# Optimization experiments

Hardware: AMD Instinct MI355X
Metric: run time of the kernel (lower is better)

Reference implementation:

```python
import jax, jax.numpy as jnp
import numpy as np
import math

NUM_LAYERS = 2
NUM_HEADS = 8
D_MODEL = 256
D_FF = 4 * D_MODEL
FACTOR = 5
B, L, F_IN = 8, 2048, 32


def layer_norm(x, g, b, eps=1e-5):
    m = x.mean(-1, keepdims=True)
    v = ((x - m) ** 2).mean(-1, keepdims=True)
    return (x - m) * jax.lax.rsqrt(v + eps) * g + b


def prob_attention(q, k, v, idx):
    # q,k,v: [B,H,L,Dh]; idx: [L,S] sampled key indices per query (ProbSparse)
    Bq, H, Lq, Dh = q.shape
    u = min(FACTOR * math.ceil(math.log(Lq)), Lq)  # number of 'active' queries
    k_s = k[:, :, idx, :]                              # [B,H,L,S,Dh] gathered keys
    qk_s = jnp.einsum('bhld,bhlsd->bhls', q, k_s)      # sampled scores
    M = qk_s.max(-1) - qk_s.sum(-1) / Lq               # sparsity measure [B,H,L]
    _, top = jax.lax.top_k(M, u)                       # [B,H,u] active query idx
    q_red = jnp.take_along_axis(q, top[..., None], axis=2)   # [B,H,u,Dh]
    scores = jnp.einsum('bhud,bhld->bhul', q_red, k) * (1.0 / math.sqrt(Dh))
    attn = jax.nn.softmax(scores, axis=-1)             # [B,H,u,L]
    upd = jnp.einsum('bhul,bhld->bhud', attn, v)       # [B,H,u,Dh]
    # initial context = mean of V (mask_flag=False), then scatter active rows
    ctx = jnp.broadcast_to(v.mean(2, keepdims=True), (Bq, H, Lq, Dh))
    bi = jnp.arange(Bq)[:, None, None]
    hi = jnp.arange(H)[None, :, None]
    return ctx.at[bi, hi, top].set(upd)


def setup_inputs() -> dict:
    key = jax.random.key(0)
    ks = jax.random.split(key, 16)
    S = min(FACTOR * math.ceil(math.log(L)), L)  # 40
    std = 0.02

    def w(k, shape):
        return jax.random.normal(k, shape, jnp.float32) * std

    inp = {}
    inp['x'] = jax.random.normal(ks[0], (B, L, F_IN), jnp.float32)
    inp['idx_sample'] = jax.random.randint(ks[1], (NUM_LAYERS, L, S), 0, L)
    inp['w_in'] = w(ks[2], (F_IN, D_MODEL)); inp['b_in'] = jnp.zeros((D_MODEL,), jnp.float32)
    inp['wq'] = w(ks[3], (NUM_LAYERS, D_MODEL, D_MODEL)); inp['bq'] = jnp.zeros((NUM_LAYERS, D_MODEL), jnp.float32)
    inp['wk'] = w(ks[4], (NUM_LAYERS, D_MODEL, D_MODEL)); inp['bk'] = jnp.zeros((NUM_LAYERS, D_MODEL), jnp.float32)
    inp['wv'] = w(ks[5], (NUM_LAYERS, D_MODEL, D_MODEL)); inp['bv'] = jnp.zeros((NUM_LAYERS, D_MODEL), jnp.float32)
    inp['wo'] = w(ks[6], (NUM_LAYERS, D_MODEL, D_MODEL)); inp['bo'] = jnp.zeros((NUM_LAYERS, D_MODEL), jnp.float32)
    inp['w_ff1'] = w(ks[7], (NUM_LAYERS, D_MODEL, D_FF)); inp['b_ff1'] = jnp.zeros((NUM_LAYERS, D_FF), jnp.float32)
    inp['w_ff2'] = w(ks[8], (NUM_LAYERS, D_FF, D_MODEL)); inp['b_ff2'] = jnp.zeros((NUM_LAYERS, D_MODEL), jnp.float32)
    inp['ln1_g'] = jnp.ones((NUM_LAYERS, D_MODEL), jnp.float32); inp['ln1_b'] = jnp.zeros((NUM_LAYERS, D_MODEL), jnp.float32)
    inp['ln2_g'] = jnp.ones((NUM_LAYERS, D_MODEL), jnp.float32); inp['ln2_b'] = jnp.zeros((NUM_LAYERS, D_MODEL), jnp.float32)
    inp['w_fc1'] = w(ks[9], (D_MODEL, 64)); inp['b_fc1'] = jnp.zeros((64,), jnp.float32)
    inp['w_fc2'] = w(ks[10], (64, 1)); inp['b_fc2'] = jnp.zeros((1,), jnp.float32)
    return inp


def reference(x, idx_sample, w_in, b_in, wq, bq, wk, bk, wv, bv, wo, bo,
              w_ff1, b_ff1, w_ff2, b_ff2, ln1_g, ln1_b, ln2_g, ln2_b,
              w_fc1, b_fc1, w_fc2, b_fc2):
    Bx, Lx, _ = x.shape
    h = x @ w_in + b_in  # [B,L,D_MODEL]
    for i in range(NUM_LAYERS):
        q = (h @ wq[i] + bq[i]).reshape(Bx, Lx, NUM_HEADS, -1).transpose(0, 2, 1, 3)
        k = (h @ wk[i] + bk[i]).reshape(Bx, Lx, NUM_HEADS, -1).transpose(0, 2, 1, 3)
        v = (h @ wv[i] + bv[i]).reshape(Bx, Lx, NUM_HEADS, -1).transpose(0, 2, 1, 3)
        ctx = prob_attention(q, k, v, idx_sample[i])            # [B,H,L,Dh]
        ctx = ctx.transpose(0, 2, 1, 3).reshape(Bx, Lx, D_MODEL)
        new_x = ctx @ wo[i] + bo[i]
        h = layer_norm(h + new_x, ln1_g[i], ln1_b[i])
        y = jax.nn.relu(h @ w_ff1[i] + b_ff1[i]) @ w_ff2[i] + b_ff2[i]
        h = layer_norm(h + y, ln2_g[i], ln2_b[i])
    last = h[:, -1, :]                      # take final time step
    out = jax.nn.relu(last @ w_fc1 + b_fc1) @ w_fc2 + b_fc2
    return out[:, None, :]                  # unsqueeze(1) -> [B,1,output_size]
```

## Files before the change

kernel.cpp:

```cpp
#include <hip/hip_runtime.h>
#include <math.h>

#define BB 8
#define LL 2048
#define DM 256
#define NH 8
#define DH 32
#define DFF 1024
#define SS 40
#define UU 40
#define BL (BB*LL)
#define NSL 8

#define SCP 260
#define KP  40
#define VP  34

typedef unsigned short ushort_t;
typedef unsigned char uchar_t;
typedef __attribute__((ext_vector_type(8))) short short8;
typedef __attribute__((ext_vector_type(4))) float f32x4;

__device__ inline ushort_t f2b(float f)
{
    unsigned int u = __float_as_uint(f);
    u += 0x7fff + ((u >> 16) & 1);
    return (ushort_t)(u >> 16);
}

__device__ inline float blo(unsigned int u) { return __uint_as_float(u << 16); }
__device__ inline float bhi(unsigned int u) { return __uint_as_float(u & 0xffff0000u); }

__device__ inline void gload16(const void* g, const void* l)
{
    __builtin_amdgcn_global_load_lds(
        (const __attribute__((address_space(1))) unsigned int*)g,
        (__attribute__((address_space(3))) unsigned int*)l, 16, 0, 0);
}

template<int RELU, int OUT_MODE>
__global__ __launch_bounds__(256)
void gemm_mfma(const ushort_t* __restrict__ A, const ushort_t* __restrict__ Bt,
               const float* __restrict__ bias, void* __restrict__ Cout,
               void* __restrict__ aux, int M, int N, int K)
{
    __shared__ ushort_t Asl[128 * 32];
    __shared__ ushort_t Bsl[128 * 32];

    const int t    = threadIdx.x;
    const int lane = t & 63;
    const int wv   = t >> 6;
    const int row0 = blockIdx.x * 128;
    const int col0 = blockIdx.y * 128;
    const int wr   = (wv >> 1) * 64;
    const int wc   = (wv & 1) * 64;
    const int quad = lane >> 4;
    const int l16  = lane & 15;

    f32x4 acc[4][4];
    #pragma unroll
    for (int i = 0; i < 4; ++i)
        #pragma unroll
        for (int j = 0; j < 4; ++j)
            acc[i][j] = 0.f;

    for (int k0 = 0; k0 < K; k0 += 32) {
        __syncthreads();
        #pragma unroll
        for (int r = 0; r < 2; ++r) {
            int g = r * 256 + t;
            const ushort_t* ga = A  + (size_t)(row0 + (g >> 2)) * K + k0 + (g & 3) * 8;
            const ushort_t* gb = Bt + (size_t)(col0 + (g >> 2)) * K + k0 + (g & 3) * 8;
            int lbase = (r * 256 + wv * 64) * 16;
            gload16(ga, (const char*)Asl + lbase);
            gload16(gb, (const char*)Bsl + lbase);
        }
        __syncthreads();

        short8 af[4], bfr[4];
        #pragma unroll
        for (int mi = 0; mi < 4; ++mi)
            af[mi] = *(const short8*)&Asl[(wr + mi * 16 + l16) * 32 + quad * 8];
        #pragma unroll
        for (int ni = 0; ni < 4; ++ni)
            bfr[ni] = *(const short8*)&Bsl[(wc + ni * 16 + l16) * 32 + quad * 8];
        #pragma unroll
        for (int mi = 0; mi < 4; ++mi)
            #pragma unroll
            for (int ni = 0; ni < 4; ++ni)
                acc[mi][ni] = __builtin_amdgcn_mfma_f32_16x16x32_bf16(
                    af[mi], bfr[ni], acc[mi][ni], 0, 0, 0);
    }

    #pragma unroll
    for (int mi = 0; mi < 4; ++mi) {
        #pragma unroll
        for (int ni = 0; ni < 4; ++ni) {
            int col = col0 + wc + ni * 16 + l16;
            float bb = bias[col];
            #pragma unroll
            for (int r = 0; r < 4; ++r) {
                int row = row0 + wr + mi * 16 + quad * 4 + r;
                float v = acc[mi][ni][r] + bb;
                if (RELU) v = v > 0.f ? v : 0.f;
                if (OUT_MODE == 0) {
                    ((float*)Cout)[(size_t)row * N + col] = v;
                } else if (OUT_MODE == 1) {
                    int tensor = col >> 8;
                    int c2 = col & 255;
                    int b  = row >> 11, l = row & (LL - 1);
                    int hh = c2 >> 5,  dh = c2 & 31;
                    int bh = b * NH + hh;
                    size_t bi = (((size_t)bh * LL + l) << 5) + dh;
                    ushort_t vb16 = f2b(v);
                    ((ushort_t*)Cout)[(size_t)tensor * (BB*NH*LL*DH) + bi] = vb16;
                    if (tensor == 1)
                        ((ushort_t*)aux)[(((size_t)l << 6) + bh) * 32 + dh] = vb16;
                } else if (OUT_MODE == 2) {
                    ((ushort_t*)Cout)[(size_t)row * N + col] = f2b(v);
                } else {
                    ((float*)Cout)[(size_t)row * N + col] = v;
                    ((ushort_t*)aux)[(size_t)row * N + col] = f2b(v);
                }
            }
        }
    }
}

template<int HEAD>
__global__ __launch_bounds__(256)
void gemmln_k(const ushort_t* __restrict__ A, const ushort_t* __restrict__ Bt,
              const float* __restrict__ bias, float* __restrict__ h,
              ushort_t* __restrict__ hb, const float* __restrict__ g,
              const float* __restrict__ beta, int K,
              const float* __restrict__ w1, const float* __restrict__ b1,
              const float* __restrict__ w2, const float* __restrict__ b2,
              float* __restrict__ out)
{
    __shared__ ushort_t Asl[2][64 * 32];
    __shared__ ushort_t Bsl[2][256 * 32];
    __shared__ float rs[4][64], rs2[4][64];
    __shared__ float hrowS[256];

    const int t    = threadIdx.x;
    const int lane = t & 63;
    const int wv   = t >> 6;
    const int row0 = blockIdx.x * 64;
    const int wc   = wv * 64;
    const int quad = lane >> 4;
    const int l16  = lane & 15;

    f32x4 acc[4][4];
    #pragma unroll
    for (int i = 0; i < 4; ++i)
        #pragma unroll
        for (int j = 0; j < 4; ++j)
            acc[i][j] = 0.f;

    auto stage = [&](int bf, int k0) {
        const ushort_t* ga = A + (size_t)(row0 + (t >> 2)) * K + k0 + (t & 3) * 8;
        gload16(ga, (const char*)Asl[bf] + wv * 1024);
        #pragma unroll
        for (int r = 0; r < 4; ++r) {
            int gg = r * 256 + t;
            const ushort_t* gb = Bt + (size_t)(gg >> 2) * K + k0 + (gg & 3) * 8;
            gload16(gb, (const char*)Bsl[bf] + (r * 256 + wv * 64) * 16);
        }
    };

    const int NS = K >> 5;
    stage(0, 0);
    __syncthreads();

    for (int ks = 0; ks < NS; ++ks) {
        int cur = ks & 1;
        if (ks + 1 < NS)
            stage(cur ^ 1, (ks + 1) << 5);

        short8 af[4], bfr[4];
        #pragma unroll
        for (int mi = 0; mi < 4; ++mi)
            af[mi] = *(const short8*)&Asl[cur][(mi * 16 + l16) * 32 + quad * 8];
        #pragma unroll
        for (int ni = 0; ni < 4; ++ni)
            bfr[ni] = *(const short8*)&Bsl[cur][(wc + ni * 16 + l16) * 32 + quad * 8];
        #pragma unroll
        for (int mi = 0; mi < 4; ++mi)
            #pragma unroll
            for (int ni = 0; ni < 4; ++ni)
                acc[mi][ni] = __builtin_amdgcn_mfma_f32_16x16x32_bf16(
                    af[mi], bfr[ni], acc[mi][ni], 0, 0, 0);

        __syncthreads();
    }

    float gcol[4], bcol[4], bic[4];
    #pragma unroll
    for (int ni = 0; ni < 4; ++ni) {
        int col = wc + ni * 16 + l16;
        gcol[ni] = g[col];
        bcol[ni] = beta[col];
        bic[ni]  = bias[col];
    }
    float ps[4][4], ps2[4][4];
    #pragma unroll
    for (int mi = 0; mi < 4; ++mi) {
        #pragma unroll
        for (int r = 0; r < 4; ++r) {
            int row = row0 + mi * 16 + quad * 4 + r;
            float s = 0.f, s2 = 0.f;
            #pragma unroll
            for (int ni = 0; ni < 4; ++ni) {
                int col = wc + ni * 16 + l16;
                float v = acc[mi][ni][r] + bic[ni] + h[(size_t)row * DM + col];
                acc[mi][ni][r] = v;
                s += v;
                s2 += v * v;
            }
            ps[mi][r] = s;
            ps2[mi][r] = s2;
        }
    }
    #pragma unroll
    for (int off = 1; off < 16; off <<= 1) {
        #pragma unroll
        for (int mi = 0; mi < 4; ++mi)
            #pragma unroll
            for (int r = 0; r < 4; ++r) {
                ps[mi][r]  += __shfl_xor(ps[mi][r],  off, 16);
                ps2[mi][r] += __shfl_xor(ps2[mi][r], off, 16);
            }
    }
    if (l16 == 0) {
        #pragma unroll
        for (int mi = 0; mi < 4; ++mi)
            #pragma unroll
            for (int r = 0; r < 4; ++r) {
                int lrow = mi * 16 + quad * 4 + r;
                rs[wv][lrow]  = ps[mi][r];
                rs2[wv][lrow] = ps2[mi][r];
            }
    }
    __syncthreads();

    #pragma unroll
    for (int mi = 0; mi < 4; ++mi) {
        #pragma unroll
        for (int r = 0; r < 4; ++r) {
            int lrow = mi * 16 + quad * 4 + r;
            int row  = row0 + lrow;
            float tot  = rs[0][lrow] + rs[1][lrow] + rs[2][lrow] + rs[3][lrow];
            float tot2 = rs2[0][lrow] + rs2[1][lrow] + rs2[2][lrow] + rs2[3][lrow];
            float mean = tot * (1.f / (float)DM);
            float var  = tot2 * (1.f / (float)DM) - mean * mean;
            float inv  = 1.0f / sqrtf(var + 1e-5f);
            #pragma unroll
            for (int ni = 0; ni < 4; ++ni) {
                int col = wc + ni * 16 + l16;
                float val = (acc[mi][ni][r] - mean) * inv * gcol[ni] + bcol[ni];
                h[(size_t)row * DM + col]  = val;
                hb[(size_t)row * DM + col] = f2b(val);
                if (HEAD && lrow == 63) hrowS[col] = val;
            }
        }
    }

    if (HEAD) {
        __syncthreads();
        if ((blockIdx.x & 31) == 31 && t < 64) {
            int b = blockIdx.x >> 5;
            float s = 0.f;
            for (int kk = 0; kk < DM; ++kk)
                s = fmaf(hrowS[kk], w1[kk * 64 + t], s);
            s += b1[t];
            s = s > 0.f ? s : 0.f;
            float contrib = s * w2[t];
            #pragma unroll
            for (int off = 32; off > 0; off >>= 1)
                contrib += __shfl_down(contrib, off, 64);
            if (t == 0) out[b] = contrib + b2[0];
        }
    }
}

__device__ inline void tcvt_dev(float (*tile)[33], const float* __restrict__ src,
                                ushort_t* __restrict__ dst, int K, int N,
                                int matStride, int bi)
{
    int tilesN = N >> 5;
    int tpm = (K >> 5) * tilesN;
    int m   = bi / tpm;
    int tid = bi % tpm;
    int k0 = (tid / tilesN) << 5, n0 = (tid % tilesN) << 5;
    const float* s = src + (size_t)m * K * N;
    ushort_t*    d = dst + (size_t)m * matStride;
    int r = threadIdx.x >> 5, c = threadIdx.x & 31;
    #pragma unroll
    for (int i = 0; i < 4; ++i)
        tile[r + 8 * i][c] = s[(size_t)(k0 + r + 8 * i) * N + n0 + c];
    __syncthreads();
    #pragma unroll
    for (int i = 0; i < 4; ++i)
        d[(size_t)(n0 + r + 8 * i) * K + k0 + c] = f2b(tile[c][r + 8 * i]);
}

__global__ __launch_bounds__(256)
void preproc_k(const float* __restrict__ wq, const float* __restrict__ wk,
               const float* __restrict__ wv, const float* __restrict__ wo,
               const float* __restrict__ wf1, const float* __restrict__ wf2,
               const float* __restrict__ w_in,
               const float* __restrict__ bq, const float* __restrict__ bk,
               const float* __restrict__ bv, const float* __restrict__ x,
               ushort_t* __restrict__ wqkvT, ushort_t* __restrict__ woT,
               ushort_t* __restrict__ wf1T, ushort_t* __restrict__ wf2T,
               ushort_t* __restrict__ w_inT, float* __restrict__ bqkv,
               ushort_t* __restrict__ xb16)
{
    __shared__ float tile[32][33];
    int b = blockIdx.x;
    if (b < 512) {
        int which = b >> 7, lb = b & 127;
        const float* src = which == 0 ? wq : which == 1 ? wk : which == 2 ? wv : wo;
        ushort_t* dst = which == 0 ? wqkvT : which == 1 ? wqkvT + 65536
                       : which == 2 ? wqkvT + 131072 : woT;
        int stride = which == 3 ? 65536 : 768 * 256;
        tcvt_dev(tile, src, dst, DM, DM, stride, lb);
    } else if (b < 1024) {
        tcvt_dev(tile, wf1, wf1T, DM, DFF, 1024 * 256, b - 512);
    } else if (b < 1536) {
        tcvt_dev(tile, wf2, wf2T, DFF, DM, 256 * 1024, b - 1024);
    } else if (b < 1544) {
        tcvt_dev(tile, w_in, w_inT, 32, DM, 256 * 32, b - 1536);
    } else if (b < 1550) {
        int t = (b - 1544) * 256 + threadIdx.x;
        int i = t / 768, j = t % 768;
        const float* s = j < 256 ? bq : (j < 512 ? bk : bv);
        bqkv[t] = s[i * 256 + (j & 255)];
    } else {
        int tid = (b - 1550) * 256 + threadIdx.x;
        float4 v = ((const float4*)x)[tid];
        unsigned int lo = f2b(v.x) | ((unsigned int)f2b(v.y) << 16);
        unsigned int hi = f2b(v.z) | ((unsigned int)f2b(v.w) << 16);
        ((uint2*)xb16)[tid] = make_uint2(lo, hi);
    }
}

__global__ __launch_bounds__(256)
void metric2_k(const ushort_t* __restrict__ qb16, const ushort_t* __restrict__ kT,
               const int* __restrict__ idx, float* __restrict__ Mout,
               unsigned int* __restrict__ jidx32)
{
    __shared__ float mst[64][5];
    int t = threadIdx.x;
    int w = t >> 6, lane = t & 63;
    int l = blockIdx.x * 4 + w;

    if (t < 64) {
        int zb = t >> 3, sel = t & 7;
        int zl = blockIdx.x * 4 + (sel >> 1), half = sel & 1;
        jidx32[(size_t)(zb * LL + zl) * 2 + half] = 0;
    }

    float4 q[8];
    {
        const uint4* qr4 = (const uint4*)(qb16 + ((size_t)(lane * LL + l) << 5));
        #pragma unroll
        for (int i = 0; i < 4; ++i) {
            uint4 u = qr4[i];
            q[2 * i]     = make_float4(blo(u.x), bhi(u.x), blo(u.y), bhi(u.y));
            q[2 * i + 1] = make_float4(blo(u.z), bhi(u.z), blo(u.w), bhi(u.w));
        }
    }

    int r40 = idx[l * SS + (lane < SS ? lane : SS - 1)];

    float mx = -3e38f, sm = 0.f;
    for (int s = 0; s < SS; ++s) {
        int r = __shfl(r40, s, 64);
        const uint4* kr = (const uint4*)(kT + (((size_t)r << 6) + lane) * 32);
        float d = 0.f;
        #pragma unroll
        for (int ww = 0; ww < 4; ++ww) {
            uint4 kv = kr[ww];
            float4 qa = q[2 * ww], qb2 = q[2 * ww + 1];
            d = fmaf(blo(kv.x), qa.x, d);
            d = fmaf(bhi(kv.x), qa.y, d);
            d = fmaf(blo(kv.y), qa.z, d);
            d = fmaf(bhi(kv.y), qa.w, d);
            d = fmaf(blo(kv.z), qb2.x, d);
            d = fmaf(bhi(kv.z), qb2.y, d);
            d = fmaf(blo(kv.w), qb2.z, d);
            d = fmaf(bhi(kv.w), qb2.w, d);
        }
        mx = fmaxf(mx, d);
        sm += d;
    }
    mst[lane][w] = mx - sm * (1.0f / (float)LL);
    __syncthreads();

    int bh = t >> 2, ls = t & 3;
    Mout[(size_t)bh * LL + blockIdx.x * 4 + ls] = mst[bh][ls];
}

__global__ __launch_bounds__(512)
void topkf_k(const float* __restrict__ Mout, int* __restrict__ top,
             uchar_t* __restrict__ jidx)
{
    __shared__ float cvS[320];
    __shared__ int   ciS[320];
    int bh = blockIdx.x;
    int t  = threadIdx.x;
    int lane = t & 63, w = t >> 6;
    int l0 = w << 8;

    float v[4];
    #pragma unroll
    for (int i = 0; i < 4; ++i)
        v[i] = Mout[(size_t)bh * LL + l0 + i * 64 + lane];

    for (int r = 0; r < UU; ++r) {
        float bv = -3e38f; int bi = 1 << 30;
        #pragma unroll
        for (int i = 0; i < 4; ++i) {
            int idx = l0 + i * 64 + lane;
            if (v[i] > bv || (v[i] == bv && idx < bi)) { bv = v[i]; bi = idx; }
        }
        #pragma unroll
        for (int off = 32; off > 0; off >>= 1) {
            float ov = __shfl_down(bv, off, 64);
            int   oi = __shfl_down(bi, off, 64);
            if (ov > bv || (ov == bv && oi < bi)) { bv = ov; bi = oi; }
        }
        bv = __shfl(bv, 0, 64);
        bi = __shfl(bi, 0, 64);
        if (lane == 0) { cvS[w * UU + r] = bv; ciS[w * UU + r] = bi; }
        int rel = bi - l0;
        if ((rel & 63) == lane) v[rel >> 6] = -3e38f;
    }
    __syncthreads();

    for (int c = t; c < 320; c += 512) {
        float mv = cvS[c]; int mi = ciS[c];
        int rank = 0;
        for (int j = 0; j < 320; ++j)
            rank += (cvS[j] > mv) || (cvS[j] == mv && ciS[j] < mi);
        if (rank < UU) {
            top[bh * UU + rank] = mi;
            int b = bh >> 3, hh = bh & 7;
            jidx[(size_t)(b * LL + mi) * 8 + hh] = (uchar_t)(rank + 1);
        }
    }
}

__global__ __launch_bounds__(256)
void attnupd_k(const ushort_t* __restrict__ qb16, const ushort_t* __restrict__ kb16,
               const ushort_t* __restrict__ vb16, const int* __restrict__ top,
               float* __restrict__ mP, float* __restrict__ sP,
               float* __restrict__ OP, float* __restrict__ vmeanP)
{
    __shared__ ushort_t qs[48 * KP];
    __shared__ ushort_t kv[256 * KP];
    __shared__ float    sc[48 * SCP];
    __shared__ float    msh[UU];
    __shared__ float    red[8][32];

    int blk = blockIdx.x;
    int sl  = blk & (NSL - 1);
    int bh  = blk >> 3;
    int t   = threadIdx.x;
    int l0  = sl << 8;
    int lane = t & 63, wvx = t >> 6;
    int quad = lane >> 4, l16 = lane & 15;
    const float scale = 0.17677669529663687f;

    for (int i = t; i < 48 * 32; i += 256) {
        int j = i >> 5, dd = i & 31;
        qs[(i >> 5) * KP + dd] = (j < UU)
            ? qb16[((size_t)(bh * LL + top[bh * UU + j]) << 5) + dd] : (ushort_t)0;
    }
    {
        const unsigned int* krow =
            (const unsigned int*)(kb16 + ((size_t)(bh * LL + l0 + t) << 5));
        #pragma unroll
        for (int i = 0; i < 16; ++i)
            ((unsigned int*)kv)[t * (KP / 2) + i] = krow[i];
    }
    __syncthreads();

    {
        short8 afq[3];
        #pragma unroll
        for (int mt = 0; mt < 3; ++mt)
            afq[mt] = *(const short8*)&qs[(mt * 16 + l16) * KP + quad * 8];
        #pragma unroll
        for (int n4 = 0; n4 < 4; ++n4) {
            int nt = wvx * 4 + n4;
            short8 bk = *(const short8*)&kv[(nt * 16 + l16) * KP + quad * 8];
            #pragma unroll
            for (int mt = 0; mt < 3; ++mt) {
                f32x4 dd = {0.f, 0.f, 0.f, 0.f};
                dd = __builtin_amdgcn_mfma_f32_16x16x32_bf16(afq[mt], bk, dd, 0, 0, 0);
                #pragma unroll
                for (int r = 0; r < 4; ++r)
                    sc[(mt * 16 + quad * 4 + r) * SCP + nt * 16 + l16] = dd[r] * scale;
            }
        }
    }
    __syncthreads();

    int j8 = t >> 5, d = t & 31;
    #pragma unroll
    for (int g = 0; g < 5; ++g) {
        int j = g * 8 + j8;
        float4 a = *(const float4*)&sc[j * SCP + 4 * d];
        float4 b = *(const float4*)&sc[j * SCP + 128 + 4 * d];
        float m = fmaxf(fmaxf(fmaxf(a.x, a.y), fmaxf(a.z, a.w)),
                        fmaxf(fmaxf(b.x, b.y), fmaxf(b.z, b.w)));
        #pragma unroll
        for (int off = 16; off > 0; off >>= 1)
            m = fmaxf(m, __shfl_down(m, off, 64));
        if (d == 0) msh[j] = m;
    }
    __syncthreads();

    #pragma unroll 2
    for (int i = t; i < UU * 64; i += 256) {
        int j = i >> 6;
        float* p = &sc[j * SCP + (i & 63) * 4];
        float4 e = *(float4*)p;
        float mm = msh[j];
        e.x = __expf(e.x - mm); e.y = __expf(e.y - mm);
        e.z = __expf(e.z - mm); e.w = __expf(e.w - mm);
        *(float4*)p = e;
    }
    __syncthreads();

    int pq = bh * NSL + sl;

    #pragma unroll
    for (int g = 0; g < 5; ++g) {
        int j = g * 8 + j8;
        float4 a = *(const float4*)&sc[j * SCP + 4 * d];
        float4 b = *(const float4*)&sc[j * SCP + 128 + 4 * d];
        float s = a.x + a.y + a.z + a.w + b.x + b.y + b.z + b.w;
        #pragma unroll
        for (int off = 16; off > 0; off >>= 1)
            s += __shfl_down(s, off, 64);
        if (d == 0) { sP[pq * UU + j] = s; mP[pq * UU + j] = msh[j]; }
    }
    {
        const unsigned int* vrow =
            (const unsigned int*)(vb16 + ((size_t)(bh * LL + l0 + t) << 5));
        #pragma unroll
        for (int i = 0; i < 16; ++i)
            *(unsigned int*)&kv[t * VP + 2 * i] = vrow[i];
        const ushort_t* base = vb16 + ((size_t)(bh * LL + l0 + j8 * 32) << 5) + d;
        float s = 0.f;
        #pragma unroll 8
        for (int i = 0; i < 32; ++i)
            s += __uint_as_float((unsigned int)base[(size_t)i << 5] << 16);
        red[j8][d] = s;
    }
    __syncthreads();

    if (t < 32) {
        float tot = 0.f;
        #pragma unroll
        for (int p = 0; p < 8; ++p) tot += red[p][t];
        vmeanP[pq * 32 + t] = tot;
    }

    if (wvx < 3) {
        f32x4 acc0 = {0.f, 0.f, 0.f, 0.f};
        f32x4 acc1 = {0.f, 0.f, 0.f, 0.f};
        #pragma unroll
        for (int ks = 0; ks < 8; ++ks) {
            float4 p0 = *(const float4*)&sc[(wvx * 16 + l16) * SCP + ks * 32 + quad * 8];
            float4 p1 = *(const float4*)&sc[(wvx * 16 + l16) * SCP + ks * 32 + quad * 8 + 4];
            short8 af;
            af[0] = (short)f2b(p0.x); af[1] = (short)f2b(p0.y);
            af[2] = (short)f2b(p0.z); af[3] = (short)f2b(p0.w);
            af[4] = (short)f2b(p1.x); af[5] = (short)f2b(p1.y);
            af[6] = (short)f2b(p1.z); af[7] = (short)f2b(p1.w);
            #pragma unroll
            for (int nt = 0; nt < 2; ++nt) {
                short8 bf;
                #pragma unroll
                for (int jj = 0; jj < 8; ++jj)
                    bf[jj] = (short)kv[(ks * 32 + quad * 8 + jj) * VP + nt * 16 + l16];
                if (nt == 0)
                    acc0 = __builtin_amdgcn_mfma_f32_16x16x32_bf16(af, bf, acc0, 0, 0, 0);
                else
                    acc1 = __builtin_amdgcn_mfma_f32_16x16x32_bf16(af, bf, acc1, 0, 0, 0);
            }
        }
        #pragma unroll
        for (int r = 0; r < 4; ++r) {
            int j = wvx * 16 + quad * 4 + r;
            if (j < UU) {
                OP[((size_t)pq * UU + j) * 32 + l16]      = acc0[r];
                OP[((size_t)pq * UU + j) * 32 + 16 + l16] = acc1[r];
            }
        }
    }
}

__global__ __launch_bounds__(256)
void fillcomb_k(const float* __restrict__ vmeanP, const uchar_t* __restrict__ jidx,
                const float* __restrict__ mP, const float* __restrict__ sP,
                const float* __restrict__ OP, ushort_t* __restrict__ ctxb)
{
    int tid = blockIdx.x * 256 + threadIdx.x;
    int pr   = tid & 127;
    int rowi = tid >> 7;
    int b    = rowi >> 11;
    int hh   = pr >> 4;
    int bh   = b * 8 + hh;
    int d0   = (pr * 2) & 31;
    int j    = (int)jidx[(size_t)rowi * 8 + hh];

    float v0, v1;
    if (j == 0) {
        float s0 = 0.f, s1 = 0.f;
        #pragma unroll
        for (int q = 0; q < NSL; ++q) {
            s0 += vmeanP[(bh * NSL + q) * 32 + d0];
            s1 += vmeanP[(bh * NSL + q) * 32 + d0 + 1];
        }
        v0 = s0 * (1.f / (float)LL);
        v1 = s1 * (1.f / (float)LL);
    } else {
        int jj = j - 1;
        float M = -3e38f;
        #pragma unroll
        for (int q = 0; q < NSL; ++q) M = fmaxf(M, mP[(bh * NSL + q) * UU + jj]);
        float S = 0.f, O0 = 0.f, O1 = 0.f;
        #pragma unroll
        for (int q = 0; q < NSL; ++q) {
            float wgt = __expf(mP[(bh * NSL + q) * UU + jj] - M);
            S  = fmaf(sP[(bh * NSL + q) * UU + jj], wgt, S);
            O0 = fmaf(OP[((size_t)(bh * NSL + q) * UU + jj) * 32 + d0], wgt, O0);
            O1 = fmaf(OP[((size_t)(bh * NSL + q) * UU + jj) * 32 + d0 + 1], wgt, O1);
        }
        v0 = O0 / S;
        v1 = O1 / S;
    }
    ((unsigned int*)ctxb)[tid] = (unsigned int)f2b(v0) | ((unsigned int)f2b(v1) << 16);
}

extern "C" void kernel_launch(void* const* d_in, const int* in_sizes, int n_in,
                              void* d_out, int out_size, void* d_ws, size_t ws_size,
                              hipStream_t stream)
{
    const float* x    = (const float*)d_in[0];
    const int*   idx  = (const int*)  d_in[1];
    const float* w_in = (const float*)d_in[2];
    const float* b_in = (const float*)d_in[3];
    const float* wq   = (const float*)d_in[4];
    const float* bq   = (const float*)d_in[5];
    const float* wk   = (const float*)d_in[6];
    const float* bk   = (const float*)d_in[7];
    const float* wv   = (const float*)d_in[8];
    const float* bv   = (const float*)d_in[9];
    const float* wo   = (const float*)d_in[10];
    const float* bo   = (const float*)d_in[11];
    const float* wf1  = (const float*)d_in[12];
    const float* bf1  = (const float*)d_in[13];
    const float* wf2  = (const float*)d_in[14];
    const float* bf2  = (const float*)d_in[15];
    const float* g1   = (const float*)d_in[16];
    const float* be1  = (const float*)d_in[17];
    const float* g2   = (const float*)d_in[18];
    const float* be2  = (const float*)d_in[19];
    const float* wfc1 = (const float*)d_in[20];
    const float* bfc1 = (const float*)d_in[21];
    const float* wfc2 = (const float*)d_in[22];
    const float* bfc2 = (const float*)d_in[23];
    float* out = (float*)d_out;

    float* ws = (float*)d_ws;
    float*    h     = ws;
    ushort_t* q16   = (ushort_t*)(ws + 4194304);
    ushort_t* k16   = q16 + 4194304;
    ushort_t* v16   = q16 + 8388608;
    ushort_t* ctxb  = q16;
    ushort_t* ffbb  = (ushort_t*)(ws + 6291456);
    float*    attnS = ws + 16777216;
    ushort_t* kT16  = (ushort_t*)attnS;
    float*    Mbuf  = attnS + 2097152;
    float*    vmeP  = attnS + 2269184;
    float*    OP    = attnS + 2285568;
    float*    mP    = attnS + 2940928;
    float*    sP    = attnS + 2961408;
    uchar_t*  jidx  = (uchar_t*)(attnS + 2981888);
    float*    scr   = ws + 20971520;
    ushort_t* xb16  = (ushort_t*)scr;
    int*      top   = (int*)(scr + 264192);
    ushort_t* hb    = (ushort_t*)(scr + 266752);
    ushort_t* wqkvT = (ushort_t*)(scr + 2363904);
    ushort_t* woT   = (ushort_t*)(scr + 2560512);
    ushort_t* wf1T  = (ushort_t*)(scr + 2626048);
    ushort_t* wf2T  = (ushort_t*)(scr + 2888192);
    ushort_t* w_inT = (ushort_t*)(scr + 3150336);
    float*    bqkv  = scr + 3154432;

    dim3 blk(256);

    preproc_k<<<dim3(2062), blk, 0, stream>>>(
        wq, wk, wv, wo, wf1, wf2, w_in, bq, bk, bv, x,
        wqkvT, woT, wf1T, wf2T, w_inT, bqkv, xb16);

    gemm_mfma<0,3><<<dim3(BL/128, 2), blk, 0, stream>>>(
        xb16, w_inT, b_in, (void*)h, (void*)hb, BL, DM, 32);

    for (int i = 0; i < 2; ++i) {
        gemm_mfma<0,1><<<dim3(BL/128, 6), blk, 0, stream>>>(
            hb, wqkvT + (size_t)i*768*256, bqkv + i*768, (void*)q16, (void*)kT16,
            BL, 768, DM);

        metric2_k<<<dim3(512), blk, 0, stream>>>(
            q16, kT16, idx + (size_t)i*LL*SS, Mbuf, (unsigned int*)jidx);
        topkf_k<<<dim3(BB*NH), dim3(512), 0, stream>>>(Mbuf, top, jidx);
        attnupd_k<<<dim3(BB*NH*NSL), blk, 0, stream>>>(q16, k16, v16, top, mP, sP, OP, vmeP);
        fillcomb_k<<<dim3(BL*DM/512), blk, 0, stream>>>(vmeP, jidx, mP, sP, OP, ctxb);

        gemmln_k<0><<<dim3(BL/64), blk, 0, stream>>>(
            ctxb, woT + (size_t)i*256*256, bo + i*DM, h, hb,
            g1 + i*DM, be1 + i*DM, DM,
            nullptr, nullptr, nullptr, nullptr, nullptr);

        gemm_mfma<1,2><<<dim3(BL/128, 8), blk, 0, stream>>>(
            hb, wf1T + (size_t)i*1024*256, bf1 + i*DFF, (void*)ffbb, nullptr, BL, DFF, DM);

        if (i == 1) {
            gemmln_k<1><<<dim3(BL/64), blk, 0, stream>>>(
                ffbb, wf2T + (size_t)i*256*1024, bf2 + i*DM, h, hb,
                g2 + i*DM, be2 + i*DM, DFF,
                wfc1, bfc1, wfc2, bfc2, out);
        } else {
            gemmln_k<0><<<dim3(BL/64), blk, 0, stream>>>(
                ffbb, wf2T + (size_t)i*256*1024, bf2 + i*DM, h, hb,
                g2 + i*DM, be2 + i*DM, DFF,
                nullptr, nullptr, nullptr, nullptr, nullptr);
        }
    }
}
```

Before: 471.8 us.

## Replace LDS-staged GEMM+LayerNorm with direct global loads across 8 waves

Rewrites the fused GEMM+LayerNorm kernel to drop the double-buffered LDS staging and its per-step barriers. Each wave now reads its A and B fragments straight from global memory into MFMA registers. The block grows to 512 threads so each of 8 waves owns 32 output columns, with the row-statistics reduction widened to 8 partials. This trades LDS traffic and synchronisation for redundant A-tile loads across waves and less coalesced 16-byte strided global reads that must be served by the caches.

Result: slower. 537.9 us (+14.0%).

```diff
diff --git a/kernel.cpp b/kernel.cpp
--- a/kernel.cpp
+++ b/kernel.cpp
@@ -128,7 +128,7 @@
 }
 
 template<int HEAD>
-__global__ __launch_bounds__(256)
+__global__ __launch_bounds__(512)
 void gemmln_k(const ushort_t* __restrict__ A, const ushort_t* __restrict__ Bt,
               const float* __restrict__ bias, float* __restrict__ h,
               ushort_t* __restrict__ hb, const float* __restrict__ g,
@@ -137,66 +137,53 @@
               const float* __restrict__ w2, const float* __restrict__ b2,
               float* __restrict__ out)
 {
-    __shared__ ushort_t Asl[2][64 * 32];
-    __shared__ ushort_t Bsl[2][256 * 32];
-    __shared__ float rs[4][64], rs2[4][64];
+    __shared__ float rs[8][64], rs2[8][64];
     __shared__ float hrowS[256];
 
     const int t    = threadIdx.x;
     const int lane = t & 63;
     const int wv   = t >> 6;
     const int row0 = blockIdx.x * 64;
-    const int wc   = wv * 64;
+    const int wc   = wv * 32;
     const int quad = lane >> 4;
     const int l16  = lane & 15;
 
-    f32x4 acc[4][4];
+    f32x4 acc[4][2];
     #pragma unroll
     for (int i = 0; i < 4; ++i)
         #pragma unroll
-        for (int j = 0; j < 4; ++j)
+        for (int j = 0; j < 2; ++j)
             acc[i][j] = 0.f;
 
-    auto stage = [&](int bf, int k0) {
-        const ushort_t* ga = A + (size_t)(row0 + (t >> 2)) * K + k0 + (t & 3) * 8;
-        gload16(ga, (const char*)Asl[bf] + wv * 1024);
-        #pragma unroll
-        for (int r = 0; r < 4; ++r) {
-            int gg = r * 256 + t;
-            const ushort_t* gb = Bt + (size_t)(gg >> 2) * K + k0 + (gg & 3) * 8;
-            gload16(gb, (const char*)Bsl[bf] + (r * 256 + wv * 64) * 16);
-        }
-    };
-
-    const int NS = K >> 5;
-    stage(0, 0);
-    __syncthreads();
-
-    for (int ks = 0; ks < NS; ++ks) {
-        int cur = ks & 1;
-        if (ks + 1 < NS)
-            stage(cur ^ 1, (ks + 1) << 5);
-
-        short8 af[4], bfr[4];
+    const ushort_t* pa[4];
+    const ushort_t* pb[2];
+    #pragma unroll
+    for (int mi = 0; mi < 4; ++mi)
+        pa[mi] = A + (size_t)(row0 + mi * 16 + l16) * K + quad * 8;
+    #pragma unroll
+    for (int ni = 0; ni < 2; ++ni)
+        pb[ni] = Bt + (size_t)(wc + ni * 16 + l16) * K + quad * 8;
+
+    #pragma unroll 4
+    for (int k0 = 0; k0 < K; k0 += 32) {
+        short8 af[4], bfr[2];
         #pragma unroll
         for (int mi = 0; mi < 4; ++mi)
-            af[mi] = *(const short8*)&Asl[cur][(mi * 16 + l16) * 32 + quad * 8];
-        #pragma unroll
-        for (int ni = 0; ni < 4; ++ni)
-            bfr[ni] = *(const short8*)&Bsl[cur][(wc + ni * 16 + l16) * 32 + quad * 8];
+            af[mi] = *(const short8*)(pa[mi] + k0);
+        #pragma unroll
+        for (int ni = 0; ni < 2; ++ni)
+            bfr[ni] = *(const short8*)(pb[ni] + k0);
         #pragma unroll
         for (int mi = 0; mi < 4; ++mi)
             #pragma unroll
-            for (int ni = 0; ni < 4; ++ni)
+            for (int ni = 0; ni < 2; ++ni)
                 acc[mi][ni] = __builtin_amdgcn_mfma_f32_16x16x32_bf16(
                     af[mi], bfr[ni], acc[mi][ni], 0, 0, 0);
-
-        __syncthreads();
-    }
-
-    float gcol[4], bcol[4], bic[4];
-    #pragma unroll
-    for (int ni = 0; ni < 4; ++ni) {
+    }
+
+    float gcol[2], bcol[2], bic[2];
+    #pragma unroll
+    for (int ni = 0; ni < 2; ++ni) {
         int col = wc + ni * 16 + l16;
         gcol[ni] = g[col];
         bcol[ni] = beta[col];
@@ -210,7 +197,7 @@
             int row = row0 + mi * 16 + quad * 4 + r;
             float s = 0.f, s2 = 0.f;
             #pragma unroll
-            for (int ni = 0; ni < 4; ++ni) {
+            for (int ni = 0; ni < 2; ++ni) {
                 int col = wc + ni * 16 + l16;
                 float v = acc[mi][ni][r] + bic[ni] + h[(size_t)row * DM + col];
                 acc[mi][ni][r] = v;
@@ -249,13 +236,17 @@
         for (int r = 0; r < 4; ++r) {
             int lrow = mi * 16 + quad * 4 + r;
             int row  = row0 + lrow;
-            float tot  = rs[0][lrow] + rs[1][lrow] + rs[2][lrow] + rs[3][lrow];
-            float tot2 = rs2[0][lrow] + rs2[1][lrow] + rs2[2][lrow] + rs2[3][lrow];
+            float tot = 0.f, tot2 = 0.f;
+            #pragma unroll
+            for (int w8 = 0; w8 < 8; ++w8) {
+                tot  += rs[w8][lrow];
+                tot2 += rs2[w8][lrow];
+            }
             float mean = tot * (1.f / (float)DM);
             float var  = tot2 * (1.f / (float)DM) - mean * mean;
             float inv  = 1.0f / sqrtf(var + 1e-5f);
             #pragma unroll
-            for (int ni = 0; ni < 4; ++ni) {
+            for (int ni = 0; ni < 2; ++ni) {
                 int col = wc + ni * 16 + l16;
                 float val = (acc[mi][ni][r] - mean) * inv * gcol[ni] + bcol[ni];
                 h[(size_t)row * DM + col]  = val;
@@ -724,7 +715,7 @@
         attnupd_k<<<dim3(BB*NH*NSL), blk, 0, stream>>>(q16, k16, v16, top, mP, sP, OP, vmeP);
         fillcomb_k<<<dim3(BL*DM/512), blk, 0, stream>>>(vmeP, jidx, mP, sP, OP, ctxb);
 
-        gemmln_k<0><<<dim3(BL/64), blk, 0, stream>>>(
+        gemmln_k<0><<<dim3(BL/64), dim3(512), 0, stream>>>(
             ctxb, woT + (size_t)i*256*256, bo + i*DM, h, hb,
             g1 + i*DM, be1 + i*DM, DM,
             nullptr, nullptr, nullptr, nullptr, nullptr);
@@ -733,12 +724,12 @@
             hb, wf1T + (size_t)i*1024*256, bf1 + i*DFF, (void*)ffbb, nullptr, BL, DFF, DM);
 
         if (i == 1) {
-            gemmln_k<1><<<dim3(BL/64), blk, 0, stream>>>(
+            gemmln_k<1><<<dim3(BL/64), dim3(512), 0, stream>>>(
                 ffbb, wf2T + (size_t)i*256*1024, bf2 + i*DM, h, hb,
                 g2 + i*DM, be2 + i*DM, DFF,
                 wfc1, bfc1, wfc2, bfc2, out);
         } else {
-            gemmln_k<0><<<dim3(BL/64), blk, 0, stream>>>(
+            gemmln_k<0><<<dim3(BL/64), dim3(512), 0, stream>>>(
                 ffbb, wf2T + (size_t)i*256*1024, bf2 + i*DM, h, hb,
                 g2 + i*DM, be2 + i*DM, DFF,
                 nullptr, nullptr, nullptr, nullptr, nullptr);
```
